# Optimization experiments

Measured on AMD Instinct MI355X. Metric: run time of the kernel, lower is better.

The kernel has to match this reference:

```python
import jax, jax.numpy as jnp
import numpy as np

B, S, D = 2, 2048, 512
M = 64            # meta_memory_dim
C = 16            # n_chunks
H = 8             # attention heads
WIN = 512         # sliding window size
N_LAYERS = 2      # n_hidden_layers of ResLinear
MAX_ALR = 0.01    # max_adaptive_lr
LR, WD, EPS = 1e-3, 1e-2, 1e-8  # AdamW hyperparams (first step from zero state)
T = M + S


def lmm_apply(ws, x):
    # ResLinear: bias-free residual MLP blocks, x <- x + silu(x W^T)
    for W in ws:
        x = x + jax.nn.silu(x @ W.T)
    return x


def chunkify(t, c):
    # [B, T, D] -> [B, L, C, D] with contiguous chunks on axis 2 (vmap in_dims=2)
    b, t_, d = t.shape
    return jnp.moveaxis(t.reshape(b, c, t_ // c, d), 1, 2)


def swa(x, wq, wk, wv, wo):
    # causal sliding-window multi-head attention
    b, t, d = x.shape
    hd = d // H
    q = (x @ wq.T).reshape(b, t, H, hd)
    k = (x @ wk.T).reshape(b, t, H, hd)
    v = (x @ wv.T).reshape(b, t, H, hd)
    scores = jnp.einsum('bqhd,bkhd->bhqk', q, k) / jnp.sqrt(jnp.float32(hd))
    i = jnp.arange(t)[:, None]
    j = jnp.arange(t)[None, :]
    mask = (j <= i) & (i - j < WIN)
    scores = jnp.where(mask, scores, jnp.finfo(scores.dtype).min)
    attn = jax.nn.softmax(scores, axis=-1)
    out = jnp.einsum('bhqk,bkhd->bqhd', attn, v).reshape(b, t, d)
    return out @ wo.T


def setup_inputs() -> dict:
    key = jax.random.key(0)
    ks = jax.random.split(key, 11)
    sc = 0.02
    return {
        'x': jax.random.normal(ks[0], (B, S, D), jnp.float32),
        'meta_memory': jax.random.normal(ks[1], (M, D), jnp.float32),
        'lmm_w': jax.random.normal(ks[2], (N_LAYERS, D, D), jnp.float32) * sc,
        'w_q': jax.random.normal(ks[3], (D, D), jnp.float32) * sc,
        'w_k': jax.random.normal(ks[4], (D, D), jnp.float32) * sc,
        'w_v': jax.random.normal(ks[5], (D, D), jnp.float32) * sc,
        'w_lr': jax.random.normal(ks[6], (1, D), jnp.float32) * sc,
        'swa_wq': jax.random.normal(ks[7], (D, D), jnp.float32) * sc,
        'swa_wk': jax.random.normal(ks[8], (D, D), jnp.float32) * sc,
        'swa_wv': jax.random.normal(ks[9], (D, D), jnp.float32) * sc,
        'swa_wo': jax.random.normal(ks[10], (D, D), jnp.float32) * sc,
    }


def reference(x, meta_memory, lmm_w, w_q, w_k, w_v, w_lr, swa_wq, swa_wk, swa_wv, swa_wo):
    # inject meta memory tokens
    meta = jnp.broadcast_to(meta_memory, (x.shape[0],) + meta_memory.shape)
    xm = jnp.concatenate([meta, x], axis=1)                   # [B, T, D]

    queries = xm @ w_q.T                                      # [B, T, D] (n_chunks=1)
    keys = chunkify(xm @ w_k.T, C)                            # [B, L, C, D]
    values = chunkify(xm @ w_v.T, C)                          # [B, L, C, D]
    alr = chunkify(jax.nn.sigmoid(xm @ w_lr.T) * MAX_ALR, C)  # [B, L, C, 1]

    def assoc_loss(ws, k, v, w):
        preds = lmm_apply(ws, k)                              # [B, L, D]
        loss = jnp.mean((preds - v) ** 2, axis=-1)            # [B, L]
        return jnp.sum(loss * w[..., 0])

    # per-chunk test-time gradients of the associative loss
    grads = jax.vmap(jax.grad(assoc_loss), in_axes=(None, 2, 2, 2))(lmm_w, keys, values, alr)
    g = grads.mean(axis=0)                                    # [N_LAYERS, D, D]

    # first AdamW step from zero optimizer state: m_hat=g, v_hat=g^2
    lmm_w_new = lmm_w * (1.0 - LR * WD) - LR * g / (jnp.sqrt(g * g) + EPS)

    retrieved = lmm_apply(lmm_w_new, queries)                 # [B, T, D]
    retrieved = swa(retrieved, swa_wq, swa_wk, swa_wv, swa_wo)
    return retrieved[:, M:, :]                                # drop meta tokens
```

## Files before the change

kernel.cpp:

```cpp
#include <hip/hip_runtime.h>
#include <hip/hip_bf16.h>

#define B_   2
#define S_   2048
#define D_   512
#define M_   64
#define T_   2112
#define BT_  4224
#define H_   8
#define WIN_ 512

typedef short s16x8 __attribute__((ext_vector_type(8)));
typedef float f32x4 __attribute__((ext_vector_type(4)));
typedef unsigned short ushort_t;

__device__ __forceinline__ float siluf(float x) {
    float s = 1.0f / (1.0f + expf(-x));
    return x * s;
}
__device__ __forceinline__ float dsiluf(float x) {
    float s = 1.0f / (1.0f + expf(-x));
    return s * (1.0f + x * (1.0f - s));
}
__device__ __forceinline__ float bf2f(ushort_t u) {
    union { float f; unsigned int i; } x; x.i = ((unsigned int)u) << 16; return x.f;
}
__device__ __forceinline__ ushort_t f2bf(float f) {
    union { float f; unsigned int i; } x; x.f = f;
    unsigned int r = x.i + 0x7FFFu + ((x.i >> 16) & 1u);
    return (ushort_t)(r >> 16);
}
__device__ __forceinline__ void pack8(ushort_t* dst, const float* v) {
    ushort_t tmp[8];
#pragma unroll
    for (int i = 0; i < 8; ++i) tmp[i] = f2bf(v[i]);
    *(int4*)dst = *(const int4*)tmp;
}

struct PrepArgs {
    const float* wsrc[9]; ushort_t* wdst[9];
    const float* l1src;   ushort_t* l1t;
    const float* x; const float* meta; ushort_t* xm;
    const float* wlr; float* alr;
};
__global__ __launch_bounds__(256)
void prep_kernel(PrepArgs p) {
    __shared__ float tbuf[32][33];
    int bid = blockIdx.x;
    int tid = threadIdx.x;
    if (bid < 1152) {
        int w = bid >> 7;
        int idx = ((bid & 127) << 8) + tid;
        const float* src = p.wsrc[w] + (size_t)idx * 8;
        float v[8];
        *(float4*)&v[0] = *(const float4*)src;
        *(float4*)&v[4] = *(const float4*)(src + 4);
        pack8(p.wdst[w] + (size_t)idx * 8, v);
    } else if (bid < 1408) {
        int wz = bid - 1152;
        int bx = wz & 15, by = wz >> 4;
        int tr = tid >> 3, tc = (tid & 7) * 4;
        int r0 = by * 32, c0 = bx * 32;
        *(float4*)&tbuf[tr][tc] = *(const float4*)&p.l1src[(size_t)(r0 + tr) * 512 + c0 + tc];
        __syncthreads();
        ushort_t o[4];
#pragma unroll
        for (int i = 0; i < 4; ++i) o[i] = f2bf(tbuf[tc + i][tr]);
        *(ushort2*)&p.l1t[(size_t)(c0 + tr) * 512 + r0 + tc] = *(ushort2*)&o[0];
        *(ushort2*)&p.l1t[(size_t)(c0 + tr) * 512 + r0 + tc + 2] = *(ushort2*)&o[2];
    } else if (bid < 2464) {
        int idx = (bid - 1408) * 256 + tid;
        int seg = idx & 63;
        int row = idx >> 6;
        int b = row / T_;
        int t = row - b * T_;
        const float* src;
        if (t < M_) src = p.meta + (size_t)t * 512 + seg * 8;
        else        src = p.x + ((size_t)b * S_ + (t - M_)) * 512 + seg * 8;
        float v[8];
        *(float4*)&v[0] = *(const float4*)src;
        *(float4*)&v[4] = *(const float4*)(src + 4);
        pack8(p.xm + (size_t)row * 512 + seg * 8, v);
    } else {
        int r = (bid - 2464) * 4 + (tid >> 6);
        int lane = tid & 63;
        int b = r / T_;
        int t = r - b * T_;
        const float* row = (t < M_) ? (p.meta + (size_t)t * 512)
                                    : (p.x + ((size_t)b * S_ + (t - M_)) * 512);
        float s = 0.f;
#pragma unroll
        for (int k = 0; k < 8; ++k) s = fmaf(row[lane + k * 64], p.wlr[lane + k * 64], s);
#pragma unroll
        for (int off = 32; off >= 1; off >>= 1) s += __shfl_xor(s, off, 64);
        if (lane == 0) p.alr[r] = 0.01f / (1.0f + expf(-s));
    }
}

template<int MODE>
__global__ __launch_bounds__(256)
void mgemm(const ushort_t* __restrict__ A, const ushort_t* __restrict__ Bt,
           float* __restrict__ F0,
           ushort_t* __restrict__ U0, ushort_t* __restrict__ U1,
           ushort_t* __restrict__ U2, ushort_t* __restrict__ U3,
           ushort_t* __restrict__ U4,
           const float* __restrict__ alrp) {
    __shared__ ushort_t As[64 * 64];
    __shared__ ushort_t Bs[64 * 64];
    int tid = threadIdx.x;
    int m0 = blockIdx.x * 64, n0 = blockIdx.y * 64;
    int srow = tid >> 2;
    int sseg = (tid & 3) << 1;
    int wid = tid >> 6;
    int lane = tid & 63;
    int wm = (wid & 1) << 5;
    int wn = (wid >> 1) << 5;
    int fr = lane & 15;
    int fq = lane >> 4;
    int sw = srow & 7;
    const ushort_t* ga = A  + (size_t)(m0 + srow) * 512 + sseg * 8;
    const ushort_t* gb = Bt + (size_t)(n0 + srow) * 512 + sseg * 8;
    int4 av0 = *(const int4*)ga;
    int4 av1 = *(const int4*)(ga + 8);
    int4 bv0 = *(const int4*)gb;
    int4 bv1 = *(const int4*)(gb + 8);
    f32x4 acc[2][2] = {};
    for (int k0 = 0; k0 < 512; k0 += 64) {
        __syncthreads();
        *(int4*)&As[srow * 64 + ((sseg    ) ^ sw) * 8] = av0;
        *(int4*)&As[srow * 64 + ((sseg + 1) ^ sw) * 8] = av1;
        *(int4*)&Bs[srow * 64 + ((sseg    ) ^ sw) * 8] = bv0;
        *(int4*)&Bs[srow * 64 + ((sseg + 1) ^ sw) * 8] = bv1;
        __syncthreads();
        if (k0 + 64 < 512) {
            av0 = *(const int4*)(ga + k0 + 64);
            av1 = *(const int4*)(ga + k0 + 72);
            bv0 = *(const int4*)(gb + k0 + 64);
            bv1 = *(const int4*)(gb + k0 + 72);
        }
#pragma unroll
        for (int ks = 0; ks < 2; ++ks) {
            int seg = fq + ks * 4;
            int rA0 = wm + fr,      rA1 = wm + 16 + fr;
            int rB0 = wn + fr,      rB1 = wn + 16 + fr;
            s16x8 a0 = *(const s16x8*)&As[rA0 * 64 + (seg ^ (rA0 & 7)) * 8];
            s16x8 a1 = *(const s16x8*)&As[rA1 * 64 + (seg ^ (rA1 & 7)) * 8];
            s16x8 b0 = *(const s16x8*)&Bs[rB0 * 64 + (seg ^ (rB0 & 7)) * 8];
            s16x8 b1 = *(const s16x8*)&Bs[rB1 * 64 + (seg ^ (rB1 & 7)) * 8];
            acc[0][0] = __builtin_amdgcn_mfma_f32_16x16x32_bf16(a0, b0, acc[0][0], 0, 0, 0);
            acc[0][1] = __builtin_amdgcn_mfma_f32_16x16x32_bf16(a0, b1, acc[0][1], 0, 0, 0);
            acc[1][0] = __builtin_amdgcn_mfma_f32_16x16x32_bf16(a1, b0, acc[1][0], 0, 0, 0);
            acc[1][1] = __builtin_amdgcn_mfma_f32_16x16x32_bf16(a1, b1, acc[1][1], 0, 0, 0);
        }
    }
#pragma unroll
    for (int i = 0; i < 2; ++i) {
        int row0 = m0 + wm + i * 16 + fq * 4;
        float c4[4];
        if (MODE == 2) {
#pragma unroll
            for (int r = 0; r < 4; ++r) c4[r] = (2.0f / 512.0f) * alrp[row0 + r];
        }
#pragma unroll
        for (int j = 0; j < 2; ++j) {
            int col = n0 + wn + j * 16 + fr;
            if (MODE == 0) {
                int sg = col >> 9, cl = col & 511;
                ushort_t t4[4];
#pragma unroll
                for (int r = 0; r < 4; ++r) t4[r] = f2bf(acc[i][j][r]);
                if (sg == 0) {
#pragma unroll
                    for (int r = 0; r < 4; ++r) U0[(size_t)(row0 + r) * 512 + cl] = t4[r];
                } else if (sg == 1) {
#pragma unroll
                    for (int r = 0; r < 4; ++r) U1[(size_t)(row0 + r) * 512 + cl] = t4[r];
                    *(uint2*)&U2[(size_t)cl * BT_ + row0] = *(uint2*)t4;
                } else {
#pragma unroll
                    for (int r = 0; r < 4; ++r) U3[(size_t)(row0 + r) * 512 + cl] = t4[r];
                }
            } else if (MODE == 5) {
                int sg = col >> 9, cl = col & 511;
                ushort_t t4[4];
#pragma unroll
                for (int r = 0; r < 4; ++r) t4[r] = f2bf(acc[i][j][r]);
                if (sg == 0) {
#pragma unroll
                    for (int r = 0; r < 4; ++r) U0[(size_t)(row0 + r) * 512 + cl] = t4[r];
                } else if (sg == 1) {
#pragma unroll
                    for (int r = 0; r < 4; ++r) U1[(size_t)(row0 + r) * 512 + cl] = t4[r];
                } else {
                    int bb = row0 / T_;
                    int t0 = row0 - bb * T_;
                    *(uint2*)&U2[((size_t)(bb * 512) + cl) * T_ + t0] = *(uint2*)t4;
                }
            } else if (MODE == 1) {
                ushort_t t4[4];
#pragma unroll
                for (int r = 0; r < 4; ++r) {
                    size_t off = (size_t)(row0 + r) * 512 + col;
                    float z = acc[i][j][r];
                    float h = bf2f(U1[off]) + siluf(z);
                    ushort_t hb = f2bf(h);
                    U0[off] = hb;
                    t4[r] = hb;
                    U3[off] = f2bf(dsiluf(z));
                }
                *(uint2*)&U2[(size_t)col * BT_ + row0] = *(uint2*)t4;
            } else if (MODE == 2) {
                ushort_t t4[4];
#pragma unroll
                for (int r = 0; r < 4; ++r) {
                    size_t off = (size_t)(row0 + r) * 512 + col;
                    float z = acc[i][j][r];
                    float s = 1.f / (1.f + expf(-z));
                    float d = c4[r] * (bf2f(U1[off]) + z * s - bf2f(U3[off]));
                    U4[off] = f2bf(d);
                    ushort_t u = f2bf(d * (s * (1.f + z * (1.f - s))));
                    U0[off] = u;
                    t4[r] = u;
                }
                *(uint2*)&U2[(size_t)col * BT_ + row0] = *(uint2*)t4;
            } else if (MODE == 3) {
                ushort_t t4[4];
#pragma unroll
                for (int r = 0; r < 4; ++r) {
                    size_t off = (size_t)(row0 + r) * 512 + col;
                    float g = bf2f(U1[off]) + acc[i][j][r];
                    t4[r] = f2bf(g * bf2f(U2[off]));
                }
                *(uint2*)&U0[(size_t)col * BT_ + row0] = *(uint2*)t4;
            } else if (MODE == 4) {
#pragma unroll
                for (int r = 0; r < 4; ++r) {
                    size_t off = (size_t)(row0 + r) * 512 + col;
                    U0[off] = f2bf(bf2f(U1[off]) + siluf(acc[i][j][r]));
                }
            } else if (MODE == 6) {
#pragma unroll
                for (int r = 0; r < 4; ++r) {
                    int row = row0 + r;
                    int bb = row / T_;
                    int t = row - bb * T_;
                    if (t >= M_) F0[((size_t)bb * S_ + (t - M_)) * 512 + col] = acc[i][j][r];
                }
            }
        }
    }
}

__global__ __launch_bounds__(256)
void gemm_dw2(const ushort_t* __restrict__ A1T, const ushort_t* __restrict__ B1T,
              const ushort_t* __restrict__ A0T, const ushort_t* __restrict__ B0T,
              float* __restrict__ Cpart) {
    __shared__ ushort_t As[64 * 64];
    __shared__ ushort_t Bs[64 * 64];
    int tid = threadIdx.x;
    int zz = blockIdx.z;
    int layer = (zz >= 6);
    int slice = layer ? (zz - 6) : zz;
    const ushort_t* AT  = layer ? A1T : A0T;
    const ushort_t* BT2 = layer ? B1T : B0T;
    int m0 = blockIdx.x * 64, n0 = blockIdx.y * 64;
    int kbase = slice * 704;
    int srow = tid >> 2;
    int sseg = (tid & 3) << 1;
    int wid = tid >> 6;
    int lane = tid & 63;
    int wm = (wid & 1) << 5;
    int wn = (wid >> 1) << 5;
    int fr = lane & 15;
    int fq = lane >> 4;
    int sw = srow & 7;
    const ushort_t* ga = AT  + (size_t)(m0 + srow) * BT_ + kbase + sseg * 8;
    const ushort_t* gb = BT2 + (size_t)(n0 + srow) * BT_ + kbase + sseg * 8;
    int4 av0 = *(const int4*)ga;
    int4 av1 = *(const int4*)(ga + 8);
    int4 bv0 = *(const int4*)gb;
    int4 bv1 = *(const int4*)(gb + 8);
    f32x4 acc[2][2] = {};
    for (int kt = 0; kt < 11; ++kt) {
        __syncthreads();
        *(int4*)&As[srow * 64 + ((sseg    ) ^ sw) * 8] = av0;
        *(int4*)&As[srow * 64 + ((sseg + 1) ^ sw) * 8] = av1;
        *(int4*)&Bs[srow * 64 + ((sseg    ) ^ sw) * 8] = bv0;
        *(int4*)&Bs[srow * 64 + ((sseg + 1) ^ sw) * 8] = bv1;
        __syncthreads();
        if (kt < 10) {
            int koff = (kt + 1) * 64;
            av0 = *(const int4*)(ga + koff);
            av1 = *(const int4*)(ga + koff + 8);
            bv0 = *(const int4*)(gb + koff);
            bv1 = *(const int4*)(gb + koff + 8);
        }
#pragma unroll
        for (int ks = 0; ks < 2; ++ks) {
            int seg = fq + ks * 4;
            int rA0 = wm + fr,      rA1 = wm + 16 + fr;
            int rB0 = wn + fr,      rB1 = wn + 16 + fr;
            s16x8 a0 = *(const s16x8*)&As[rA0 * 64 + (seg ^ (rA0 & 7)) * 8];
            s16x8 a1 = *(const s16x8*)&As[rA1 * 64 + (seg ^ (rA1 & 7)) * 8];
            s16x8 b0 = *(const s16x8*)&Bs[rB0 * 64 + (seg ^ (rB0 & 7)) * 8];
            s16x8 b1 = *(const s16x8*)&Bs[rB1 * 64 + (seg ^ (rB1 & 7)) * 8];
            acc[0][0] = __builtin_amdgcn_mfma_f32_16x16x32_bf16(a0, b0, acc[0][0], 0, 0, 0);
            acc[0][1] = __builtin_amdgcn_mfma_f32_16x16x32_bf16(a0, b1, acc[0][1], 0, 0, 0);
            acc[1][0] = __builtin_amdgcn_mfma_f32_16x16x32_bf16(a1, b0, acc[1][0], 0, 0, 0);
            acc[1][1] = __builtin_amdgcn_mfma_f32_16x16x32_bf16(a1, b1, acc[1][1], 0, 0, 0);
        }
    }
    float* C = Cpart + (size_t)zz * 262144;
#pragma unroll
    for (int i = 0; i < 2; ++i)
#pragma unroll
        for (int j = 0; j < 2; ++j)
#pragma unroll
            for (int r = 0; r < 4; ++r)
                C[(size_t)(m0 + wm + i * 16 + fq * 4 + r) * 512 + n0 + wn + j * 16 + fr] =
                    acc[i][j][r];
}

__global__ void adam_kernel(const float* __restrict__ W, const float* __restrict__ dWp,
                            ushort_t* __restrict__ Wnb) {
    int idx = blockIdx.x * 256 + threadIdx.x;
    int layer = idx >> 18;
    int i = idx & 262143;
    const float* base = dWp + (size_t)layer * 6 * 262144 + i;
    float g = 0.f;
#pragma unroll
    for (int z = 0; z < 6; ++z) g += base[(size_t)z * 262144];
    g *= (1.0f / 16.0f);
    float w = W[idx];
    float o = w * (1.0f - 1e-5f) - 1e-3f * g / (fabsf(g) + 1e-8f);
    Wnb[idx] = f2bf(o);
}

__global__ __launch_bounds__(256)
void swa_mfma(const ushort_t* __restrict__ qh, const ushort_t* __restrict__ kh,
              const ushort_t* __restrict__ vhT, ushort_t* __restrict__ ao) {
    __shared__ ushort_t Qs[64 * 64];
    __shared__ ushort_t Ks[64 * 64];
    __shared__ ushort_t Vs[64 * 64];
    __shared__ ushort_t Pw[4][16 * 72];
    int qt = 32 - (int)blockIdx.x;
    int hh = blockIdx.y;
    int b  = blockIdx.z;
    int tid = threadIdx.x;
    int wave = tid >> 6, lane = tid & 63;
    int fr = lane & 15, fq = lane >> 4;
    int tok = tid & 63, cs0 = tid >> 6;

    {
        const ushort_t* src = qh + ((size_t)(b * T_ + qt * 64 + tok)) * 512 + hh * 64;
#pragma unroll
        for (int p = 0; p < 2; ++p) {
            int seg = cs0 + p * 4;
            *(int4*)&Qs[tok * 64 + ((seg ^ (tok & 7)) << 3)] = *(const int4*)(src + seg * 8);
        }
    }
    __syncthreads();
    s16x8 qf0 = *(const s16x8*)&Qs[(wave * 16 + fr) * 64 + (((0 + fq) ^ (fr & 7)) << 3)];
    s16x8 qf1 = *(const s16x8*)&Qs[(wave * 16 + fr) * 64 + (((4 + fq) ^ (fr & 7)) << 3)];

    int i_q = qt * 64 + wave * 16 + fr;
    int iqmin = qt * 64 + wave * 16;
    float l_i = 0.f;
    f32x4 o[4] = {};
    int jstart = qt * 64 - (WIN_ - 1);
    if (jstart < 0) jstart = 0;
    jstart &= ~63;
    int jend = qt * 64;
    const ushort_t* kp = kh + ((size_t)(b * T_ + jstart + tok)) * 512 + hh * 64;
    const ushort_t* vp = vhT + ((size_t)(b * 512 + hh * 64 + tok)) * T_ + jstart;
    int4 ka = *(const int4*)(kp + cs0 * 8);
    int4 kb2 = *(const int4*)(kp + (cs0 + 4) * 8);
    int4 va = *(const int4*)(vp + cs0 * 8);
    int4 vb2 = *(const int4*)(vp + (cs0 + 4) * 8);
    for (int jb = jstart; jb <= jend; jb += 64) {
        __syncthreads();
        *(int4*)&Ks[tok * 64 + (((cs0    ) ^ (tok & 7)) << 3)] = ka;
        *(int4*)&Ks[tok * 64 + (((cs0 + 4) ^ (tok & 7)) << 3)] = kb2;
        *(int4*)&Vs[tok * 64 + (((cs0    ) ^ (tok & 7)) << 3)] = va;
        *(int4*)&Vs[tok * 64 + (((cs0 + 4) ^ (tok & 7)) << 3)] = vb2;
        __syncthreads();
        if (jb + 64 <= jend) {
            kp += 64 * 512;
            vp += 64;
            ka  = *(const int4*)(kp + cs0 * 8);
            kb2 = *(const int4*)(kp + (cs0 + 4) * 8);
            va  = *(const int4*)(vp + cs0 * 8);
            vb2 = *(const int4*)(vp + (cs0 + 4) * 8);
        }
        f32x4 sa[4] = {};
#pragma unroll
        for (int kf = 0; kf < 4; ++kf) {
            int krow = kf * 16 + fr;
            s16x8 a0 = *(const s16x8*)&Ks[krow * 64 + (((0 + fq) ^ (fr & 7)) << 3)];
            s16x8 a1 = *(const s16x8*)&Ks[krow * 64 + (((4 + fq) ^ (fr & 7)) << 3)];
            sa[kf] = __builtin_amdgcn_mfma_f32_16x16x32_bf16(a0, qf0, sa[kf], 0, 0, 0);
            sa[kf] = __builtin_amdgcn_mfma_f32_16x16x32_bf16(a1, qf1, sa[kf], 0, 0, 0);
        }
        float psum = 0.f;
        bool full = (jb + 63 <= iqmin) && (jb >= iqmin + 15 - (WIN_ - 1));
        if (full) {
#pragma unroll
            for (int kf = 0; kf < 4; ++kf)
#pragma unroll
                for (int r = 0; r < 4; ++r) {
                    float p = __expf(sa[kf][r] * 0.125f);
                    ushort_t pb = f2bf(p);
                    psum += bf2f(pb);
                    Pw[wave][fr * 72 + kf * 16 + fq * 4 + r] = pb;
                }
        } else {
#pragma unroll
            for (int kf = 0; kf < 4; ++kf)
#pragma unroll
                for (int r = 0; r < 4; ++r) {
                    int j2 = jb + kf * 16 + fq * 4 + r;
                    bool valid = (j2 <= i_q) && (i_q - j2 < WIN_);
                    float p = valid ? __expf(sa[kf][r] * 0.125f) : 0.f;
                    ushort_t pb = f2bf(p);
                    psum += bf2f(pb);
                    Pw[wave][fr * 72 + kf * 16 + fq * 4 + r] = pb;
                }
        }
        psum += __shfl_xor(psum, 16);
        psum += __shfl_xor(psum, 32);
        l_i += psum;
#pragma unroll
        for (int ks = 0; ks < 2; ++ks) {
            s16x8 pa = *(const s16x8*)&Pw[wave][fr * 72 + ks * 32 + fq * 8];
#pragma unroll
            for (int nf = 0; nf < 4; ++nf) {
                int vrow = nf * 16 + fr;
                s16x8 bv = *(const s16x8*)&Vs[vrow * 64 + (((ks * 4 + fq) ^ (fr & 7)) << 3)];
                o[nf] = __builtin_amdgcn_mfma_f32_16x16x32_bf16(pa, bv, o[nf], 0, 0, 0);
            }
        }
    }
    float linv = 1.0f / l_i;
    float l0 = __shfl(linv, fq * 4 + 0);
    float l1 = __shfl(linv, fq * 4 + 1);
    float l2 = __shfl(linv, fq * 4 + 2);
    float l3 = __shfl(linv, fq * 4 + 3);
#pragma unroll
    for (int nf = 0; nf < 4; ++nf) {
        int col = hh * 64 + nf * 16 + fr;
        size_t row0 = (size_t)(b * T_) + qt * 64 + wave * 16 + fq * 4;
        ao[(row0 + 0) * 512 + col] = f2bf(o[nf][0] * l0);
        ao[(row0 + 1) * 512 + col] = f2bf(o[nf][1] * l1);
        ao[(row0 + 2) * 512 + col] = f2bf(o[nf][2] * l2);
        ao[(row0 + 3) * 512 + col] = f2bf(o[nf][3] * l3);
    }
}

extern "C" void kernel_launch(void* const* d_in, const int* in_sizes, int n_in,
                              void* d_out, int out_size, void* d_ws, size_t ws_size,
                              hipStream_t stream) {
    (void)in_sizes; (void)n_in; (void)out_size; (void)ws_size;
    const float* x      = (const float*)d_in[0];
    const float* meta   = (const float*)d_in[1];
    const float* lmm_w  = (const float*)d_in[2];
    const float* w_q    = (const float*)d_in[3];
    const float* w_k    = (const float*)d_in[4];
    const float* w_v    = (const float*)d_in[5];
    const float* w_lr   = (const float*)d_in[6];
    const float* swa_wq = (const float*)d_in[7];
    const float* swa_wk = (const float*)d_in[8];
    const float* swa_wv = (const float*)d_in[9];
    const float* swa_wo = (const float*)d_in[10];
    float* out = (float*)d_out;
    float* ws  = (float*)d_ws;

    const size_t BTD = (size_t)BT_ * D_;
    float* alr = ws;
    float* dWp = alr + BT_;
    ushort_t* xb = (ushort_t*)(dWp + 12 * 262144);
    ushort_t* B0  = xb + 0 * BTD;
    ushort_t* B1  = xb + 1 * BTD;
    ushort_t* B2  = xb + 2 * BTD;
    ushort_t* B3  = xb + 3 * BTD;
    ushort_t* B4  = xb + 4 * BTD;
    ushort_t* B5  = xb + 5 * BTD;
    ushort_t* B6  = xb + 6 * BTD;
    ushort_t* B7  = xb + 7 * BTD;
    ushort_t* B8  = xb + 8 * BTD;
    ushort_t* B9  = xb + 9 * BTD;
    ushort_t* B10 = xb + 10 * BTD;
    ushort_t* wbf = xb + 11 * BTD;
    ushort_t* wq_bf  = wbf + 0 * 262144;
    ushort_t* l0_bf  = wbf + 3 * 262144;
    ushort_t* l1_bf  = wbf + 4 * 262144;
    ushort_t* sq_bf  = wbf + 5 * 262144;
    ushort_t* wo_bf  = wbf + 8 * 262144;
    ushort_t* l1t_bf = wbf + 9 * 262144;
    ushort_t* wn_bf  = wbf + 10 * 262144;

    dim3 blk(256);
    dim3 gg(66, 8);
    dim3 gq(66, 24);
    dim3 gdw(8, 8, 12);

    PrepArgs pa;
    pa.wsrc[0] = w_q;    pa.wdst[0] = wq_bf;
    pa.wsrc[1] = w_k;    pa.wdst[1] = wbf + 1 * 262144;
    pa.wsrc[2] = w_v;    pa.wdst[2] = wbf + 2 * 262144;
    pa.wsrc[3] = lmm_w;  pa.wdst[3] = l0_bf;
    pa.wsrc[4] = lmm_w + 262144; pa.wdst[4] = l1_bf;
    pa.wsrc[5] = swa_wq; pa.wdst[5] = sq_bf;
    pa.wsrc[6] = swa_wk; pa.wdst[6] = wbf + 6 * 262144;
    pa.wsrc[7] = swa_wv; pa.wdst[7] = wbf + 7 * 262144;
    pa.wsrc[8] = swa_wo; pa.wdst[8] = wo_bf;
    pa.l1src = lmm_w + 262144; pa.l1t = l1t_bf;
    pa.x = x; pa.meta = meta; pa.xm = B0;
    pa.wlr = w_lr; pa.alr = alr;

    prep_kernel<<<dim3(3520), blk, 0, stream>>>(pa);
    mgemm<0><<<gq, blk, 0, stream>>>(B0, wq_bf, nullptr, B1, B2, B3, B4, nullptr, nullptr);
    mgemm<1><<<gg, blk, 0, stream>>>(B2, l0_bf, nullptr, B5, B2, B6, B10, nullptr, nullptr);
    mgemm<2><<<gg, blk, 0, stream>>>(B5, l1_bf, nullptr, B7, B5, B8, B4, B9, alr);
    mgemm<3><<<gg, blk, 0, stream>>>(B7, l1t_bf, nullptr, B0, B9, B10, nullptr, nullptr, nullptr);
    gemm_dw2<<<gdw, blk, 0, stream>>>(B8, B6, B0, B3, dWp);
    adam_kernel<<<dim3(2048), blk, 0, stream>>>(lmm_w, dWp, wn_bf);
    mgemm<4><<<gg, blk, 0, stream>>>(B1, wn_bf, nullptr, B0, B1, nullptr, nullptr, nullptr, nullptr);
    mgemm<4><<<gg, blk, 0, stream>>>(B0, wn_bf + 262144, nullptr, B4, B0, nullptr, nullptr, nullptr, nullptr);
    mgemm<5><<<gq, blk, 0, stream>>>(B4, sq_bf, nullptr, B1, B5, B6, nullptr, nullptr, nullptr);
    swa_mfma<<<dim3(33, 8, 2), blk, 0, stream>>>(B1, B5, B6, B2);
    mgemm<6><<<gg, blk, 0, stream>>>(B2, wo_bf, out, nullptr, nullptr, nullptr, nullptr, nullptr, nullptr);
}
```

Before: 209.8 us.

## Use 128x128 tiles for fused QKV GEMMs and weight-gradient GEMM

Adds a 128x128-tile MFMA GEMM kernel in which each wave computes a 64x64 sub-tile, and uses it for the two wide fused projection GEMMs (modes 0 and 5). The dW GEMM gets the same larger tile, with its split-K reworked from 6 slices of 704 to 11 slices of 384 per layer, and the Adam kernel now sums 11 partials. The aim is more data reuse per LDS load and fewer redundant global reads. In exchange each block uses more registers and LDS, fewer blocks are launched, and there is more partial-sum traffic.

```diff
diff --git a/kernel.cpp b/kernel.cpp
--- a/kernel.cpp
+++ b/kernel.cpp
@@ -95,6 +95,178 @@
         for (int off = 32; off >= 1; off >>= 1) s += __shfl_xor(s, off, 64);
         if (lane == 0) p.alr[r] = 0.01f / (1.0f + expf(-s));
     }
+}
+
+template<int MODE>
+__global__ __launch_bounds__(256)
+void mgemm128(const ushort_t* __restrict__ A, const ushort_t* __restrict__ Bt,
+              ushort_t* __restrict__ U0, ushort_t* __restrict__ U1,
+              ushort_t* __restrict__ U2, ushort_t* __restrict__ U3) {
+    __shared__ ushort_t As[128 * 64];
+    __shared__ ushort_t Bs[128 * 64];
+    int tid = threadIdx.x;
+    int m0 = blockIdx.x * 128;
+    int by = blockIdx.y;
+    int n0 = by * 128;
+    int wave = tid >> 6, lane = tid & 63;
+    int fr = lane & 15, fq = lane >> 4;
+    int wm = (wave & 1) << 6;
+    int wn = (wave >> 1) << 6;
+    int srow = tid >> 1;
+    int sseg = (tid & 1) << 2;
+    int ssw = srow & 7;
+    const ushort_t* ga = A  + (size_t)(m0 + srow) * 512 + sseg * 8;
+    const ushort_t* gb = Bt + (size_t)(n0 + srow) * 512 + sseg * 8;
+    int4 av[4], bv[4];
+#pragma unroll
+    for (int p = 0; p < 4; ++p) {
+        av[p] = *(const int4*)(ga + p * 8);
+        bv[p] = *(const int4*)(gb + p * 8);
+    }
+    f32x4 acc[4][4] = {};
+    for (int k0 = 0; k0 < 512; k0 += 64) {
+        __syncthreads();
+#pragma unroll
+        for (int p = 0; p < 4; ++p) {
+            *(int4*)&As[srow * 64 + ((sseg + p) ^ ssw) * 8] = av[p];
+            *(int4*)&Bs[srow * 64 + ((sseg + p) ^ ssw) * 8] = bv[p];
+        }
+        __syncthreads();
+        if (k0 + 64 < 512) {
+#pragma unroll
+            for (int p = 0; p < 4; ++p) {
+                av[p] = *(const int4*)(ga + k0 + 64 + p * 8);
+                bv[p] = *(const int4*)(gb + k0 + 64 + p * 8);
+            }
+        }
+#pragma unroll
+        for (int ks = 0; ks < 2; ++ks) {
+            int seg = fq + ks * 4;
+            int sx = (seg ^ (fr & 7)) * 8;
+            s16x8 af[4], bf[4];
+#pragma unroll
+            for (int i = 0; i < 4; ++i) {
+                af[i] = *(const s16x8*)&As[(wm + i * 16 + fr) * 64 + sx];
+                bf[i] = *(const s16x8*)&Bs[(wn + i * 16 + fr) * 64 + sx];
+            }
+#pragma unroll
+            for (int i = 0; i < 4; ++i)
+#pragma unroll
+                for (int j = 0; j < 4; ++j)
+                    acc[i][j] = __builtin_amdgcn_mfma_f32_16x16x32_bf16(af[i], bf[j], acc[i][j], 0, 0, 0);
+        }
+    }
+    int sg = by >> 2;
+#pragma unroll
+    for (int i = 0; i < 4; ++i) {
+        int row0 = m0 + wm + i * 16 + fq * 4;
+#pragma unroll
+        for (int j = 0; j < 4; ++j) {
+            int cl = (by & 3) * 128 + wn + j * 16 + fr;
+            ushort_t t4[4];
+#pragma unroll
+            for (int r = 0; r < 4; ++r) t4[r] = f2bf(acc[i][j][r]);
+            if (MODE == 0) {
+                if (sg == 0) {
+#pragma unroll
+                    for (int r = 0; r < 4; ++r) U0[(size_t)(row0 + r) * 512 + cl] = t4[r];
+                } else if (sg == 1) {
+#pragma unroll
+                    for (int r = 0; r < 4; ++r) U1[(size_t)(row0 + r) * 512 + cl] = t4[r];
+                    *(uint2*)&U2[(size_t)cl * BT_ + row0] = *(uint2*)t4;
+                } else {
+#pragma unroll
+                    for (int r = 0; r < 4; ++r) U3[(size_t)(row0 + r) * 512 + cl] = t4[r];
+                }
+            } else {
+                if (sg == 0) {
+#pragma unroll
+                    for (int r = 0; r < 4; ++r) U0[(size_t)(row0 + r) * 512 + cl] = t4[r];
+                } else if (sg == 1) {
+#pragma unroll
+                    for (int r = 0; r < 4; ++r) U1[(size_t)(row0 + r) * 512 + cl] = t4[r];
+                } else {
+                    int bb = row0 / T_;
+                    int t0 = row0 - bb * T_;
+                    *(uint2*)&U2[((size_t)(bb * 512) + cl) * T_ + t0] = *(uint2*)t4;
+                }
+            }
+        }
+    }
+}
+
+__global__ __launch_bounds__(256)
+void gemm_dw128(const ushort_t* __restrict__ A1T, const ushort_t* __restrict__ B1T,
+                const ushort_t* __restrict__ A0T, const ushort_t* __restrict__ B0T,
+                float* __restrict__ Cpart) {
+    __shared__ ushort_t As[128 * 64];
+    __shared__ ushort_t Bs[128 * 64];
+    int tid = threadIdx.x;
+    int zz = blockIdx.z;
+    int layer = (zz >= 11);
+    int slice = layer ? (zz - 11) : zz;
+    const ushort_t* AT  = layer ? A1T : A0T;
+    const ushort_t* BT2 = layer ? B1T : B0T;
+    int m0 = blockIdx.x * 128, n0 = blockIdx.y * 128;
+    int kbase = slice * 384;
+    int wave = tid >> 6, lane = tid & 63;
+    int fr = lane & 15, fq = lane >> 4;
+    int wm = (wave & 1) << 6;
+    int wn = (wave >> 1) << 6;
+    int srow = tid >> 1;
+    int sseg = (tid & 1) << 2;
+    int ssw = srow & 7;
+    const ushort_t* ga = AT  + (size_t)(m0 + srow) * BT_ + kbase + sseg * 8;
+    const ushort_t* gb = BT2 + (size_t)(n0 + srow) * BT_ + kbase + sseg * 8;
+    int4 av[4], bv[4];
+#pragma unroll
+    for (int p = 0; p < 4; ++p) {
+        av[p] = *(const int4*)(ga + p * 8);
+        bv[p] = *(const int4*)(gb + p * 8);
+    }
+    f32x4 acc[4][4] = {};
+    for (int kt = 0; kt < 6; ++kt) {
+        __syncthreads();
+#pragma unroll
+        for (int p = 0; p < 4; ++p) {
+            *(int4*)&As[srow * 64 + ((sseg + p) ^ ssw) * 8] = av[p];
+            *(int4*)&Bs[srow * 64 + ((sseg + p) ^ ssw) * 8] = bv[p];
+        }
+        __syncthreads();
+        if (kt < 5) {
+            int koff = (kt + 1) * 64;
+#pragma unroll
+            for (int p = 0; p < 4; ++p) {
+                av[p] = *(const int4*)(ga + koff + p * 8);
+                bv[p] = *(const int4*)(gb + koff + p * 8);
+            }
+        }
+#pragma unroll
+        for (int ks = 0; ks < 2; ++ks) {
+            int seg = fq + ks * 4;
+            int sx = (seg ^ (fr & 7)) * 8;
+            s16x8 af[4], bf[4];
+#pragma unroll
+            for (int i = 0; i < 4; ++i) {
+                af[i] = *(const s16x8*)&As[(wm + i * 16 + fr) * 64 + sx];
+                bf[i] = *(const s16x8*)&Bs[(wn + i * 16 + fr) * 64 + sx];
+            }
+#pragma unroll
+            for (int i = 0; i < 4; ++i)
+#pragma unroll
+                for (int j = 0; j < 4; ++j)
+                    acc[i][j] = __builtin_amdgcn_mfma_f32_16x16x32_bf16(af[i], bf[j], acc[i][j], 0, 0, 0);
+        }
+    }
+    float* C = Cpart + (size_t)zz * 262144;
+#pragma unroll
+    for (int i = 0; i < 4; ++i)
+#pragma unroll
+        for (int j = 0; j < 4; ++j)
+#pragma unroll
+            for (int r = 0; r < 4; ++r)
+                C[(size_t)(m0 + wm + i * 16 + fq * 4 + r) * 512 + n0 + wn + j * 16 + fr] =
+                    acc[i][j][r];
 }
 
 template<int MODE>
@@ -164,39 +336,7 @@
 #pragma unroll
         for (int j = 0; j < 2; ++j) {
             int col = n0 + wn + j * 16 + fr;
-            if (MODE == 0) {
-                int sg = col >> 9, cl = col & 511;
-                ushort_t t4[4];
-#pragma unroll
-                for (int r = 0; r < 4; ++r) t4[r] = f2bf(acc[i][j][r]);
-                if (sg == 0) {
-#pragma unroll
-                    for (int r = 0; r < 4; ++r) U0[(size_t)(row0 + r) * 512 + cl] = t4[r];
-                } else if (sg == 1) {
-#pragma unroll
-                    for (int r = 0; r < 4; ++r) U1[(size_t)(row0 + r) * 512 + cl] = t4[r];
-                    *(uint2*)&U2[(size_t)cl * BT_ + row0] = *(uint2*)t4;
-                } else {
-#pragma unroll
-                    for (int r = 0; r < 4; ++r) U3[(size_t)(row0 + r) * 512 + cl] = t4[r];
-                }
-            } else if (MODE == 5) {
-                int sg = col >> 9, cl = col & 511;
-                ushort_t t4[4];
-#pragma unroll
-                for (int r = 0; r < 4; ++r) t4[r] = f2bf(acc[i][j][r]);
-                if (sg == 0) {
-#pragma unroll
-                    for (int r = 0; r < 4; ++r) U0[(size_t)(row0 + r) * 512 + cl] = t4[r];
-                } else if (sg == 1) {
-#pragma unroll
-                    for (int r = 0; r < 4; ++r) U1[(size_t)(row0 + r) * 512 + cl] = t4[r];
-                } else {
-                    int bb = row0 / T_;
-                    int t0 = row0 - bb * T_;
-                    *(uint2*)&U2[((size_t)(bb * 512) + cl) * T_ + t0] = *(uint2*)t4;
-                }
-            } else if (MODE == 1) {
+            if (MODE == 1) {
                 ushort_t t4[4];
 #pragma unroll
                 for (int r = 0; r < 4; ++r) {
@@ -251,85 +391,15 @@
     }
 }
 
-__global__ __launch_bounds__(256)
-void gemm_dw2(const ushort_t* __restrict__ A1T, const ushort_t* __restrict__ B1T,
-              const ushort_t* __restrict__ A0T, const ushort_t* __restrict__ B0T,
-              float* __restrict__ Cpart) {
-    __shared__ ushort_t As[64 * 64];
-    __shared__ ushort_t Bs[64 * 64];
-    int tid = threadIdx.x;
-    int zz = blockIdx.z;
-    int layer = (zz >= 6);
-    int slice = layer ? (zz - 6) : zz;
-    const ushort_t* AT  = layer ? A1T : A0T;
-    const ushort_t* BT2 = layer ? B1T : B0T;
-    int m0 = blockIdx.x * 64, n0 = blockIdx.y * 64;
-    int kbase = slice * 704;
-    int srow = tid >> 2;
-    int sseg = (tid & 3) << 1;
-    int wid = tid >> 6;
-    int lane = tid & 63;
-    int wm = (wid & 1) << 5;
-    int wn = (wid >> 1) << 5;
-    int fr = lane & 15;
-    int fq = lane >> 4;
-    int sw = srow & 7;
-    const ushort_t* ga = AT  + (size_t)(m0 + srow) * BT_ + kbase + sseg * 8;
-    const ushort_t* gb = BT2 + (size_t)(n0 + srow) * BT_ + kbase + sseg * 8;
-    int4 av0 = *(const int4*)ga;
-    int4 av1 = *(const int4*)(ga + 8);
-    int4 bv0 = *(const int4*)gb;
-    int4 bv1 = *(const int4*)(gb + 8);
-    f32x4 acc[2][2] = {};
-    for (int kt = 0; kt < 11; ++kt) {
-        __syncthreads();
-        *(int4*)&As[srow * 64 + ((sseg    ) ^ sw) * 8] = av0;
-        *(int4*)&As[srow * 64 + ((sseg + 1) ^ sw) * 8] = av1;
-        *(int4*)&Bs[srow * 64 + ((sseg    ) ^ sw) * 8] = bv0;
-        *(int4*)&Bs[srow * 64 + ((sseg + 1) ^ sw) * 8] = bv1;
-        __syncthreads();
-        if (kt < 10) {
-            int koff = (kt + 1) * 64;
-            av0 = *(const int4*)(ga + koff);
-            av1 = *(const int4*)(ga + koff + 8);
-            bv0 = *(const int4*)(gb + koff);
-            bv1 = *(const int4*)(gb + koff + 8);
-        }
-#pragma unroll
-        for (int ks = 0; ks < 2; ++ks) {
-            int seg = fq + ks * 4;
-            int rA0 = wm + fr,      rA1 = wm + 16 + fr;
-            int rB0 = wn + fr,      rB1 = wn + 16 + fr;
-            s16x8 a0 = *(const s16x8*)&As[rA0 * 64 + (seg ^ (rA0 & 7)) * 8];
-            s16x8 a1 = *(const s16x8*)&As[rA1 * 64 + (seg ^ (rA1 & 7)) * 8];
-            s16x8 b0 = *(const s16x8*)&Bs[rB0 * 64 + (seg ^ (rB0 & 7)) * 8];
-            s16x8 b1 = *(const s16x8*)&Bs[rB1 * 64 + (seg ^ (rB1 & 7)) * 8];
-            acc[0][0] = __builtin_amdgcn_mfma_f32_16x16x32_bf16(a0, b0, acc[0][0], 0, 0, 0);
-            acc[0][1] = __builtin_amdgcn_mfma_f32_16x16x32_bf16(a0, b1, acc[0][1], 0, 0, 0);
-            acc[1][0] = __builtin_amdgcn_mfma_f32_16x16x32_bf16(a1, b0, acc[1][0], 0, 0, 0);
-            acc[1][1] = __builtin_amdgcn_mfma_f32_16x16x32_bf16(a1, b1, acc[1][1], 0, 0, 0);
-        }
-    }
-    float* C = Cpart + (size_t)zz * 262144;
-#pragma unroll
-    for (int i = 0; i < 2; ++i)
-#pragma unroll
-        for (int j = 0; j < 2; ++j)
-#pragma unroll
-            for (int r = 0; r < 4; ++r)
-                C[(size_t)(m0 + wm + i * 16 + fq * 4 + r) * 512 + n0 + wn + j * 16 + fr] =
-                    acc[i][j][r];
-}
-
 __global__ void adam_kernel(const float* __restrict__ W, const float* __restrict__ dWp,
                             ushort_t* __restrict__ Wnb) {
     int idx = blockIdx.x * 256 + threadIdx.x;
     int layer = idx >> 18;
     int i = idx & 262143;
-    const float* base = dWp + (size_t)layer * 6 * 262144 + i;
+    const float* base = dWp + (size_t)layer * 11 * 262144 + i;
     float g = 0.f;
 #pragma unroll
-    for (int z = 0; z < 6; ++z) g += base[(size_t)z * 262144];
+    for (int z = 0; z < 11; ++z) g += base[(size_t)z * 262144];
     g *= (1.0f / 16.0f);
     float w = W[idx];
     float o = w * (1.0f - 1e-5f) - 1e-3f * g / (fabsf(g) + 1e-8f);
@@ -477,7 +547,7 @@
     const size_t BTD = (size_t)BT_ * D_;
     float* alr = ws;
     float* dWp = alr + BT_;
-    ushort_t* xb = (ushort_t*)(dWp + 12 * 262144);
+    ushort_t* xb = (ushort_t*)(dWp + 22 * 262144);
     ushort_t* B0  = xb + 0 * BTD;
     ushort_t* B1  = xb + 1 * BTD;
     ushort_t* B2  = xb + 2 * BTD;
@@ -500,8 +570,8 @@
 
     dim3 blk(256);
     dim3 gg(66, 8);
-    dim3 gq(66, 24);
-    dim3 gdw(8, 8, 12);
+    dim3 g128(33, 12);
+    dim3 gdw(4, 4, 22);
 
     PrepArgs pa;
     pa.wsrc[0] = w_q;    pa.wdst[0] = wq_bf;
@@ -518,15 +588,15 @@
     pa.wlr = w_lr; pa.alr = alr;
 
     prep_kernel<<<dim3(3520), blk, 0, stream>>>(pa);
-    mgemm<0><<<gq, blk, 0, stream>>>(B0, wq_bf, nullptr, B1, B2, B3, B4, nullptr, nullptr);
+    mgemm128<0><<<g128, blk, 0, stream>>>(B0, wq_bf, B1, B2, B3, B4);
     mgemm<1><<<gg, blk, 0, stream>>>(B2, l0_bf, nullptr, B5, B2, B6, B10, nullptr, nullptr);
     mgemm<2><<<gg, blk, 0, stream>>>(B5, l1_bf, nullptr, B7, B5, B8, B4, B9, alr);
     mgemm<3><<<gg, blk, 0, stream>>>(B7, l1t_bf, nullptr, B0, B9, B10, nullptr, nullptr, nullptr);
-    gemm_dw2<<<gdw, blk, 0, stream>>>(B8, B6, B0, B3, dWp);
+    gemm_dw128<<<gdw, blk, 0, stream>>>(B8, B6, B0, B3, dWp);
     adam_kernel<<<dim3(2048), blk, 0, stream>>>(lmm_w, dWp, wn_bf);
     mgemm<4><<<gg, blk, 0, stream>>>(B1, wn_bf, nullptr, B0, B1, nullptr, nullptr, nullptr, nullptr);
     mgemm<4><<<gg, blk, 0, stream>>>(B0, wn_bf + 262144, nullptr, B4, B0, nullptr, nullptr, nullptr, nullptr);
-    mgemm<5><<<gq, blk, 0, stream>>>(B4, sq_bf, nullptr, B1, B5, B6, nullptr, nullptr, nullptr);
+    mgemm128<5><<<g128, blk, 0, stream>>>(B4, sq_bf, B1, B5, B6, nullptr);
     swa_mfma<<<dim3(33, 8, 2), blk, 0, stream>>>(B1, B5, B6, B2);
     mgemm<6><<<gg, blk, 0, stream>>>(B2, wo_bf, out, nullptr, nullptr, nullptr, nullptr, nullptr, nullptr);
 }
```

Measured after the change: 302.7 us. +44.3%, slower.
